# Performance work log

Measured on AMD Instinct MI355X. Metric: run time of the kernel, lower is better.

The kernel has to match this reference:

```python
import jax, jax.numpy as jnp
import numpy as np

B, T, C = 4, 2048, 1024
H, HD = 16, 64          # n_heads, head_dim (C = H*HD)
R = 8                   # LoRA rank
SCALING = 16.0 / R      # alpha / r = 2.0


def setup_inputs() -> dict:
    key = jax.random.key(0)
    ks = jax.random.split(key, 16)
    std_a = 1.0 / np.sqrt(R)  # LoRA A init std (B init is zeros in torch; use randn here for a non-trivial baseline)
    inp = {
        "x":  jax.random.normal(ks[0], (B, T, C), dtype=jnp.float32),
        # per-head stacked projection weights [H, C, HD] (bias=False heads)
        "Wq": jax.random.normal(ks[1], (H, C, HD), dtype=jnp.float32) * 0.02,
        "Wk": jax.random.normal(ks[2], (H, C, HD), dtype=jnp.float32) * 0.02,
        "Wv": jax.random.normal(ks[3], (H, C, HD), dtype=jnp.float32) * 0.02,
        # per-head LoRA factors
        "Aq": jax.random.normal(ks[4], (H, C, R), dtype=jnp.float32) * std_a,
        "Bq": jax.random.normal(ks[5], (H, R, HD), dtype=jnp.float32) * 0.02,
        "Ak": jax.random.normal(ks[6], (H, C, R), dtype=jnp.float32) * std_a,
        "Bk": jax.random.normal(ks[7], (H, R, HD), dtype=jnp.float32) * 0.02,
        "Av": jax.random.normal(ks[8], (H, C, R), dtype=jnp.float32) * std_a,
        "Bv": jax.random.normal(ks[9], (H, R, HD), dtype=jnp.float32) * 0.02,
        # output projection C->C with bias, plus LoRA
        "Wp": jax.random.normal(ks[10], (C, C), dtype=jnp.float32) * 0.02,
        "bp": jnp.zeros((C,), dtype=jnp.float32),
        "Ap": jax.random.normal(ks[11], (C, R), dtype=jnp.float32) * std_a,
        "Bp": jax.random.normal(ks[12], (R, C), dtype=jnp.float32) * 0.02,
    }
    return inp


def _lora_proj(x, W, A, Bm):
    # x: [B,T,C]; W: [H,C,HD]; A: [H,C,R]; Bm: [H,R,HD] -> [B,H,T,HD]
    base = jnp.einsum('btc,hcd->bhtd', x, W)
    lora = jnp.einsum('bhtr,hrd->bhtd', jnp.einsum('btc,hcr->bhtr', x, A), Bm)
    return base + SCALING * lora


def reference(x, Wq, Wk, Wv, Aq, Bq, Ak, Bk, Av, Bv, Wp, bp, Ap, Bp):
    Bsz, Tlen, Cdim = x.shape
    q = _lora_proj(x, Wq, Aq, Bq)  # [B,H,T,HD]
    k = _lora_proj(x, Wk, Ak, Bk)
    v = _lora_proj(x, Wv, Av, Bv)

    scores = jnp.einsum('bhtd,bhsd->bhts', q, k) * (HD ** -0.5)  # [B,H,T,T]
    causal = jnp.tril(jnp.ones((Tlen, Tlen), dtype=bool))
    scores = jnp.where(causal, scores, -jnp.inf)
    weights = jax.nn.softmax(scores, axis=-1)  # dropout p=0 (eval) -> no-op

    out = jnp.einsum('bhts,bhsd->bhtd', weights, v)            # [B,H,T,HD]
    out = out.transpose(0, 2, 1, 3).reshape(Bsz, Tlen, Cdim)   # concat heads

    proj = out @ Wp + bp + SCALING * ((out @ Ap) @ Bp)
    return proj
```

## Files before the change

kernel.cpp:

```cpp
#include <hip/hip_runtime.h>
#include <hip/hip_bf16.h>
#include <stdint.h>

typedef __attribute__((ext_vector_type(4))) float f32x4;
typedef __attribute__((ext_vector_type(8))) short bf16x8;

#define LOG2E 1.44269504088896340736f

__device__ __forceinline__ unsigned short f2bf(float f) {
  union { float f; unsigned u; } c; c.f = f;
  unsigned u = c.u + 0x7FFFu + ((c.u >> 16) & 1u);
  return (unsigned short)(u >> 16);
}

__device__ __forceinline__ void gload_lds16(const void* g, void* l) {
  __builtin_amdgcn_global_load_lds((const __attribute__((address_space(1))) void*)g,
                                   (__attribute__((address_space(3))) void*)l, 16, 0, 0);
}

__global__ __launch_bounds__(256) void cast_x_kernel(const float* __restrict__ x,
                                                     unsigned short* __restrict__ o) {
  int i = blockIdx.x * 256 + threadIdx.x;
  const float4* xv = (const float4*)x;
  float4 a = xv[2 * i], b = xv[2 * i + 1];
  union { uint4 v; unsigned short s[8]; } u;
  u.s[0] = f2bf(a.x); u.s[1] = f2bf(a.y); u.s[2] = f2bf(a.z); u.s[3] = f2bf(a.w);
  u.s[4] = f2bf(b.x); u.s[5] = f2bf(b.y); u.s[6] = f2bf(b.z); u.s[7] = f2bf(b.w);
  ((uint4*)o)[i] = u.v;
}

__global__ __launch_bounds__(256) void fold_head_kernel(const float* __restrict__ W,
                                                        const float* __restrict__ A,
                                                        const float* __restrict__ Bm,
                                                        unsigned short* __restrict__ outT,
                                                        float scale) {
  int h = blockIdx.x, cb = blockIdx.y;
  __shared__ unsigned short tile[64 * 65];
  const float* Wh = W + (size_t)h * 65536;
  const float* Ah = A + (size_t)h * 8192;
  const float* Bh = Bm + (size_t)h * 512;
  int t = threadIdx.x;
  for (int i = 0; i < 16; ++i) {
    int idx = i * 256 + t;
    int cl = idx >> 6, d = idx & 63;
    int c = cb * 64 + cl;
    float acc = 0.f;
#pragma unroll
    for (int r = 0; r < 8; ++r) acc += Ah[c * 8 + r] * Bh[r * 64 + d];
    float val = scale * (Wh[c * 64 + d] + 2.0f * acc);
    tile[cl * 65 + d] = f2bf(val);
  }
  __syncthreads();
  for (int i = 0; i < 16; ++i) {
    int idx = i * 256 + t;
    int d = idx >> 6, cl = idx & 63;
    outT[(size_t)(h * 64 + d) * 1024 + cb * 64 + cl] = tile[cl * 65 + d];
  }
}

__global__ __launch_bounds__(256) void fold_proj_kernel(const float* __restrict__ W,
                                                        const float* __restrict__ A,
                                                        const float* __restrict__ Bm,
                                                        unsigned short* __restrict__ outT) {
  int nb = blockIdx.x, cb = blockIdx.y;
  __shared__ unsigned short tile[64 * 65];
  int t = threadIdx.x;
  for (int i = 0; i < 16; ++i) {
    int idx = i * 256 + t;
    int cl = idx >> 6, d = idx & 63;
    int c = cb * 64 + cl, n = nb * 64 + d;
    float acc = 0.f;
#pragma unroll
    for (int r = 0; r < 8; ++r) acc += A[c * 8 + r] * Bm[r * 1024 + n];
    float val = W[(size_t)c * 1024 + n] + 2.0f * acc;
    tile[cl * 65 + d] = f2bf(val);
  }
  __syncthreads();
  for (int i = 0; i < 16; ++i) {
    int idx = i * 256 + t;
    int d = idx >> 6, cl = idx & 63;
    outT[(size_t)(nb * 64 + d) * 1024 + cb * 64 + cl] = tile[cl * 65 + d];
  }
}

template <int MODE>
__global__ __launch_bounds__(256) void gemm_kernel(const unsigned short* __restrict__ A,
                                                   const unsigned short* __restrict__ B,
                                                   void* __restrict__ Cout,
                                                   const float* __restrict__ bias,
                                                   int M, int N, int K) {
  __shared__ unsigned short lds[8192];
  const int t = threadIdx.x;
  const int m0 = blockIdx.y * 128, n0 = blockIdx.x * 128;
  const int wid = t >> 6, lane = t & 63;
  const int wm = (wid >> 1) * 64, wn = (wid & 1) * 64;
  const int lr = lane & 15, lg = lane >> 4;
  f32x4 acc[4][4];
#pragma unroll
  for (int i = 0; i < 4; ++i)
#pragma unroll
    for (int j = 0; j < 4; ++j) acc[i][j] = (f32x4){0.f, 0.f, 0.f, 0.f};

  for (int k0 = 0; k0 < K; k0 += 32) {
#pragma unroll
    for (int ch = 0; ch < 2; ++ch) {
      int idx = ch * 256 + t;
      int row = idx >> 2, cb = (idx & 3) * 8;
      gload_lds16(A + (size_t)(m0 + row) * K + k0 + cb, &lds[idx * 8]);
    }
#pragma unroll
    for (int ch = 0; ch < 2; ++ch) {
      int idx = ch * 256 + t;
      int row = idx >> 2, cb = (idx & 3) * 8;
      gload_lds16(B + (size_t)(n0 + row) * K + k0 + cb, &lds[4096 + idx * 8]);
    }
    __syncthreads();
    bf16x8 af[4], bfr[4];
#pragma unroll
    for (int i = 0; i < 4; ++i) {
      af[i] = *(const bf16x8*)&lds[(wm + i * 16 + lr) * 32 + lg * 8];
      bfr[i] = *(const bf16x8*)&lds[4096 + (wn + i * 16 + lr) * 32 + lg * 8];
    }
#pragma unroll
    for (int i = 0; i < 4; ++i)
#pragma unroll
      for (int j = 0; j < 4; ++j)
        acc[i][j] = __builtin_amdgcn_mfma_f32_16x16x32_bf16(af[i], bfr[j], acc[i][j], 0, 0, 0);
    __syncthreads();
  }

#pragma unroll
  for (int i = 0; i < 4; ++i) {
#pragma unroll
    for (int r = 0; r < 4; ++r) {
      int row = m0 + wm + i * 16 + lg * 4 + r;
#pragma unroll
      for (int j = 0; j < 4; ++j) {
        int col = n0 + wn + j * 16 + lr;
        float v = acc[i][j][r];
        if (MODE == 0)
          ((unsigned short*)Cout)[(size_t)row * N + col] = f2bf(v);
        else
          ((float*)Cout)[(size_t)row * N + col] = v + bias[col];
      }
    }
  }
}

__global__ __launch_bounds__(256) void vtrans_kernel(const unsigned short* __restrict__ qkv,
                                                     unsigned short* __restrict__ vtb) {
  __shared__ unsigned short tile[64][66];
  const int tt = blockIdx.x, bh = blockIdx.y;
  const int b = bh >> 4, h = bh & 15;
  const size_t srcBase = ((size_t)b * 2048 + tt * 64) * 3072 + 2048 + h * 64;
  const int t = threadIdx.x;
#pragma unroll
  for (int ch = 0; ch < 2; ++ch) {
    int idx = ch * 256 + t;
    int tl = idx >> 3, c = idx & 7;
    *(uint4*)&tile[tl][c * 8] = *(const uint4*)(qkv + srcBase + (size_t)tl * 3072 + c * 8);
  }
  __syncthreads();
#pragma unroll
  for (int ch = 0; ch < 2; ++ch) {
    int idx = ch * 256 + t;
    int d = idx >> 3, tc = idx & 7;
    union { uint4 v; unsigned short s[8]; } u;
#pragma unroll
    for (int j = 0; j < 8; ++j) u.s[j] = tile[tc * 8 + j][d];
    *(uint4*)(vtb + ((size_t)bh * 64 + d) * 2048 + tt * 64 + tc * 8) = u.v;
  }
}

__global__ __launch_bounds__(256) void attn_kernel(const unsigned short* __restrict__ qkv,
                                                   const unsigned short* __restrict__ vtb,
                                                   unsigned short* __restrict__ out) {
  __shared__ __align__(16) char kl[2][8192];
  __shared__ __align__(16) char vt[2][8192];
  __shared__ __align__(16) char pl[8192];
  const int t = threadIdx.x;
  const int wid = t >> 6, lane = t & 63;
  const int lr = lane & 15, lg = lane >> 4;
  const int i = blockIdx.x;
  const int xcd = i & 7, s = i >> 3;
  const int bh = xcd + 8 * (s >> 5);
  const int qtile = 31 - (s & 31);
  const int b = bh >> 4, h = bh & 15;
  const size_t baseRow = (size_t)b * 2048;
  const int nkt = qtile + 1;
  const int q0w = qtile * 64 + wid * 16;
  char* pb = pl + wid * 2048;
  const int swP = ((lr & 1) << 4) | ((lr & 12) << 3);
  const int srow = lane >> 3;
  const int sc = lane & 7;

  const unsigned short* qp = qkv + (baseRow + q0w + lr) * 3072 + h * 64 + lg * 8;
  bf16x8 qf0 = *(const bf16x8*)qp;
  bf16x8 qf1 = *(const bf16x8*)(qp + 32);

  f32x4 acc_o[4];
#pragma unroll
  for (int d = 0; d < 4; ++d) acc_o[d] = (f32x4){0.f, 0.f, 0.f, 0.f};
  float l_acc = 0.f;

  const unsigned short* vrow = vtb + (size_t)bh * 131072;

  auto stage = [&](int kt, int buf) {
#pragma unroll
    for (int ch = 0; ch < 2; ++ch) {
      int kr = ch * 32 + wid * 8 + srow;
      int gc = sc ^ (kr & 7);
      gload_lds16(qkv + (baseRow + kt * 64 + kr) * 3072 + 1024 + h * 64 + gc * 8,
                  &kl[buf][(ch * 256 + t) * 16]);
    }
#pragma unroll
    for (int ch = 0; ch < 2; ++ch) {
      int d = ch * 32 + wid * 8 + srow;
      int gc = sc ^ (((d & 7) ^ (d >> 3)) & 7);
      gload_lds16(vrow + (size_t)d * 2048 + kt * 64 + gc * 8,
                  &vt[buf][(ch * 256 + t) * 16]);
    }
  };

  stage(0, 0);
  __syncthreads();

#pragma unroll 1
  for (int kt = 0; kt < nkt; ++kt) {
    const int cur = kt & 1;
    if (kt + 1 < nkt) stage(kt + 1, cur ^ 1);

    const char* klc = kl[cur];
    f32x4 z[4];
#pragma unroll
    for (int nt = 0; nt < 4; ++nt) {
      int key = nt * 16 + lr;
      const char* kb = klc + key * 128;
      int sw = (key & 7) << 4;
      bf16x8 kf0 = *(const bf16x8*)(kb + ((lg * 16) ^ sw));
      bf16x8 kf1 = *(const bf16x8*)(kb + ((64 + lg * 16) ^ sw));
      f32x4 zz = (f32x4){0.f, 0.f, 0.f, 0.f};
      zz = __builtin_amdgcn_mfma_f32_16x16x32_bf16(kf0, qf0, zz, 0, 0, 0);
      zz = __builtin_amdgcn_mfma_f32_16x16x32_bf16(kf1, qf1, zz, 0, 0, 0);
      z[nt] = zz;
    }
    const bool diag = (kt == qtile);
    const int qg = q0w + lr;
#pragma unroll
    for (int nt = 0; nt < 4; ++nt) {
      union { uint2 v; unsigned short us[4]; } pk;
#pragma unroll
      for (int r = 0; r < 4; ++r) {
        float pv = exp2f(z[nt][r]);
        if (diag) {
          int keyg = kt * 64 + nt * 16 + lg * 4 + r;
          pv = (keyg > qg) ? 0.f : pv;
        }
        l_acc += pv;
        pk.us[r] = f2bf(pv);
      }
      *(uint2*)(pb + lr * 128 + (((nt * 16 + lg * 4) * 2) ^ swP)) = pk.v;
    }
#pragma unroll
    for (int kk = 0; kk < 2; ++kk) {
      bf16x8 pfr = *(const bf16x8*)(pb + lr * 128 + ((kk * 64 + lg * 16) ^ swP));
#pragma unroll
      for (int dt = 0; dt < 4; ++dt) {
        int d = dt * 16 + lr;
        int swv = (((d & 7) ^ ((d >> 3) & 7)) << 4);
        bf16x8 vf = *(const bf16x8*)(vt[cur] + d * 128 + ((kk * 64 + lg * 16) ^ swv));
        acc_o[dt] = __builtin_amdgcn_mfma_f32_16x16x32_bf16(pfr, vf, acc_o[dt], 0, 0, 0);
      }
    }

    __syncthreads();
  }

  float lsum = l_acc;
  lsum += __shfl_xor(lsum, 16);
  lsum += __shfl_xor(lsum, 32);
#pragma unroll
  for (int r = 0; r < 4; ++r) {
    float inv = 1.0f / __shfl(lsum, lg * 4 + r);
    unsigned short* op = out + (baseRow + q0w + lg * 4 + r) * 1024 + h * 64;
#pragma unroll
    for (int dt = 0; dt < 4; ++dt) op[dt * 16 + lr] = f2bf(acc_o[dt][r] * inv);
  }
}

extern "C" void kernel_launch(void* const* d_in, const int* in_sizes, int n_in,
                              void* d_out, int out_size, void* d_ws, size_t ws_size,
                              hipStream_t stream) {
  const float* x = (const float*)d_in[0];
  const float* Wq = (const float*)d_in[1];
  const float* Wk = (const float*)d_in[2];
  const float* Wv = (const float*)d_in[3];
  const float* Aq = (const float*)d_in[4];
  const float* Bq = (const float*)d_in[5];
  const float* Ak = (const float*)d_in[6];
  const float* Bk = (const float*)d_in[7];
  const float* Av = (const float*)d_in[8];
  const float* Bv = (const float*)d_in[9];
  const float* Wp = (const float*)d_in[10];
  const float* bp = (const float*)d_in[11];
  const float* Ap = (const float*)d_in[12];
  const float* Bp = (const float*)d_in[13];

  unsigned short* xb = (unsigned short*)d_ws;
  unsigned short* weff = xb + 8388608;
  unsigned short* wpeff = weff + 3145728;
  unsigned short* qkvb = wpeff + 1048576;
  unsigned short* vtb = qkvb + 25165824;
  unsigned short* attb = xb;

  cast_x_kernel<<<4096, 256, 0, stream>>>(x, xb);
  dim3 fg(16, 16);
  fold_head_kernel<<<fg, 256, 0, stream>>>(Wq, Aq, Bq, weff, 0.125f * LOG2E);
  fold_head_kernel<<<fg, 256, 0, stream>>>(Wk, Ak, Bk, weff + 1048576, 1.0f);
  fold_head_kernel<<<fg, 256, 0, stream>>>(Wv, Av, Bv, weff + 2097152, 1.0f);
  fold_proj_kernel<<<fg, 256, 0, stream>>>(Wp, Ap, Bp, wpeff);

  gemm_kernel<0><<<dim3(24, 64), 256, 0, stream>>>(xb, weff, (void*)qkvb, nullptr, 8192, 3072, 1024);
  vtrans_kernel<<<dim3(32, 64), 256, 0, stream>>>(qkvb, vtb);
  attn_kernel<<<2048, 256, 0, stream>>>(qkvb, vtb, attb);
  gemm_kernel<1><<<dim3(8, 64), 256, 0, stream>>>(attb, wpeff, d_out, bp, 8192, 1024, 1024);
}
```

Measured before the change: 336.4 us.

## Use 256x256 double-buffered GEMM, compute V transposed directly, speed up weight folding

```diff
diff --git a/kernel.cpp b/kernel.cpp
--- a/kernel.cpp
+++ b/kernel.cpp
@@ -35,26 +35,30 @@
                                                         unsigned short* __restrict__ outT,
                                                         float scale) {
   int h = blockIdx.x, cb = blockIdx.y;
-  __shared__ unsigned short tile[64 * 65];
-  const float* Wh = W + (size_t)h * 65536;
-  const float* Ah = A + (size_t)h * 8192;
-  const float* Bh = Bm + (size_t)h * 512;
+  __shared__ float Bs[8][64];
+  __shared__ unsigned short tile[64][65];
   int t = threadIdx.x;
+  if (t < 128) ((float4*)&Bs[0][0])[t] = ((const float4*)(Bm + (size_t)h * 512))[t];
+  __syncthreads();
+  int cl = t >> 2;
+  int c = cb * 64 + cl;
+  int dbase = (t & 3) * 16;
+  float4 a0 = *(const float4*)(A + (size_t)h * 8192 + c * 8);
+  float4 a1 = *(const float4*)(A + (size_t)h * 8192 + c * 8 + 4);
+  const float* Wc = W + (size_t)h * 65536 + (size_t)c * 64;
+#pragma unroll
+  for (int j = 0; j < 16; ++j) {
+    int d = dbase + j;
+    float acc = a0.x * Bs[0][d] + a0.y * Bs[1][d] + a0.z * Bs[2][d] + a0.w * Bs[3][d] +
+                a1.x * Bs[4][d] + a1.y * Bs[5][d] + a1.z * Bs[6][d] + a1.w * Bs[7][d];
+    tile[cl][d] = f2bf(scale * (Wc[d] + 2.0f * acc));
+  }
+  __syncthreads();
+#pragma unroll
   for (int i = 0; i < 16; ++i) {
     int idx = i * 256 + t;
-    int cl = idx >> 6, d = idx & 63;
-    int c = cb * 64 + cl;
-    float acc = 0.f;
-#pragma unroll
-    for (int r = 0; r < 8; ++r) acc += Ah[c * 8 + r] * Bh[r * 64 + d];
-    float val = scale * (Wh[c * 64 + d] + 2.0f * acc);
-    tile[cl * 65 + d] = f2bf(val);
-  }
-  __syncthreads();
-  for (int i = 0; i < 16; ++i) {
-    int idx = i * 256 + t;
-    int d = idx >> 6, cl = idx & 63;
-    outT[(size_t)(h * 64 + d) * 1024 + cb * 64 + cl] = tile[cl * 65 + d];
+    int d = idx >> 6, c2 = idx & 63;
+    outT[(size_t)(h * 64 + d) * 1024 + cb * 64 + c2] = tile[c2][d];
   }
 }
 
@@ -63,112 +67,129 @@
                                                         const float* __restrict__ Bm,
                                                         unsigned short* __restrict__ outT) {
   int nb = blockIdx.x, cb = blockIdx.y;
-  __shared__ unsigned short tile[64 * 65];
+  __shared__ float Bs[8][64];
+  __shared__ unsigned short tile[64][65];
   int t = threadIdx.x;
+  if (t < 128) {
+    int r = t >> 4, dc = t & 15;
+    *(float4*)&Bs[r][dc * 4] = *(const float4*)(Bm + (size_t)r * 1024 + nb * 64 + dc * 4);
+  }
+  __syncthreads();
+  int cl = t >> 2;
+  int c = cb * 64 + cl;
+  int dbase = (t & 3) * 16;
+  float4 a0 = *(const float4*)(A + (size_t)c * 8);
+  float4 a1 = *(const float4*)(A + (size_t)c * 8 + 4);
+  const float* Wc = W + (size_t)c * 1024 + nb * 64;
+#pragma unroll
+  for (int j = 0; j < 16; ++j) {
+    int d = dbase + j;
+    float acc = a0.x * Bs[0][d] + a0.y * Bs[1][d] + a0.z * Bs[2][d] + a0.w * Bs[3][d] +
+                a1.x * Bs[4][d] + a1.y * Bs[5][d] + a1.z * Bs[6][d] + a1.w * Bs[7][d];
+    tile[cl][d] = f2bf(Wc[d] + 2.0f * acc);
+  }
+  __syncthreads();
+#pragma unroll
   for (int i = 0; i < 16; ++i) {
     int idx = i * 256 + t;
-    int cl = idx >> 6, d = idx & 63;
-    int c = cb * 64 + cl, n = nb * 64 + d;
-    float acc = 0.f;
-#pragma unroll
-    for (int r = 0; r < 8; ++r) acc += A[c * 8 + r] * Bm[r * 1024 + n];
-    float val = W[(size_t)c * 1024 + n] + 2.0f * acc;
-    tile[cl * 65 + d] = f2bf(val);
-  }
-  __syncthreads();
-  for (int i = 0; i < 16; ++i) {
-    int idx = i * 256 + t;
-    int d = idx >> 6, cl = idx & 63;
-    outT[(size_t)(nb * 64 + d) * 1024 + cb * 64 + cl] = tile[cl * 65 + d];
+    int d = idx >> 6, c2 = idx & 63;
+    outT[(size_t)(nb * 64 + d) * 1024 + cb * 64 + c2] = tile[c2][d];
   }
 }
 
 template <int MODE>
-__global__ __launch_bounds__(256) void gemm_kernel(const unsigned short* __restrict__ A,
-                                                   const unsigned short* __restrict__ B,
-                                                   void* __restrict__ Cout,
-                                                   const float* __restrict__ bias,
-                                                   int M, int N, int K) {
-  __shared__ unsigned short lds[8192];
+__global__ __launch_bounds__(512) void gemm256_kernel(const unsigned short* __restrict__ A,
+                                                      const unsigned short* __restrict__ B,
+                                                      void* __restrict__ Cout,
+                                                      const float* __restrict__ bias,
+                                                      int M, int N, int K) {
+  __shared__ __align__(16) unsigned short lds[2][32768];
   const int t = threadIdx.x;
-  const int m0 = blockIdx.y * 128, n0 = blockIdx.x * 128;
-  const int wid = t >> 6, lane = t & 63;
-  const int wm = (wid >> 1) * 64, wn = (wid & 1) * 64;
+  const int lane = t & 63;
+  const int wid = t >> 6;
+  const int wm = wid >> 2, wn = wid & 3;
   const int lr = lane & 15, lg = lane >> 4;
-  f32x4 acc[4][4];
-#pragma unroll
-  for (int i = 0; i < 4; ++i)
+  const int m0 = blockIdx.y * 256, n0 = blockIdx.x * 256;
+
+  f32x4 acc[8][4];
+#pragma unroll
+  for (int i = 0; i < 8; ++i)
 #pragma unroll
     for (int j = 0; j < 4; ++j) acc[i][j] = (f32x4){0.f, 0.f, 0.f, 0.f};
 
-  for (int k0 = 0; k0 < K; k0 += 32) {
-#pragma unroll
-    for (int ch = 0; ch < 2; ++ch) {
-      int idx = ch * 256 + t;
-      int row = idx >> 2, cb = (idx & 3) * 8;
-      gload_lds16(A + (size_t)(m0 + row) * K + k0 + cb, &lds[idx * 8]);
-    }
-#pragma unroll
-    for (int ch = 0; ch < 2; ++ch) {
-      int idx = ch * 256 + t;
-      int row = idx >> 2, cb = (idx & 3) * 8;
-      gload_lds16(B + (size_t)(n0 + row) * K + k0 + cb, &lds[4096 + idx * 8]);
+  const int srow = t >> 3;
+  const int schk = t & 7;
+
+  auto stage_all = [&](int buf, int kt) {
+    const int k0 = kt * 64;
+#pragma unroll
+    for (int hh = 0; hh < 4; ++hh) {
+      const unsigned short* src = (hh < 2) ? A : B;
+      const int r0 = ((hh < 2) ? m0 : n0) + (hh & 1) * 128;
+      char* dst = (char*)lds[buf] + (hh >= 2 ? 32768 : 0) + (hh & 1) * 16384;
+#pragma unroll
+      for (int i = 0; i < 2; ++i) {
+        int row = i * 64 + srow;
+        int gc = schk ^ (row & 7);
+        gload_lds16(src + (size_t)(r0 + row) * K + k0 + gc * 8, dst + i * 8192 + t * 16);
+      }
+    }
+  };
+
+  stage_all(0, 0);
+  __syncthreads();
+
+  const int NT = K >> 6;
+#pragma unroll 1
+  for (int kt = 0; kt < NT; ++kt) {
+    const int cur = kt & 1;
+    const char* Ab = (const char*)lds[cur];
+    const char* Bb = (const char*)lds[cur] + 32768;
+#pragma unroll
+    for (int p = 0; p < 4; ++p) {
+      if (p == 0 && kt + 1 < NT) stage_all(cur ^ 1, kt + 1);
+      const int mh = p >> 1, nh = p & 1;
+#pragma unroll
+      for (int kk = 0; kk < 2; ++kk) {
+        bf16x8 af[4], bfr[2];
+#pragma unroll
+        for (int fm = 0; fm < 4; ++fm) {
+          int row = wm * 128 + mh * 64 + fm * 16 + lr;
+          af[fm] = *(const bf16x8*)(Ab + row * 128 + (((kk * 4 + lg) ^ (row & 7)) * 16));
+        }
+#pragma unroll
+        for (int fn = 0; fn < 2; ++fn) {
+          int row = wn * 64 + nh * 32 + fn * 16 + lr;
+          bfr[fn] = *(const bf16x8*)(Bb + row * 128 + (((kk * 4 + lg) ^ (row & 7)) * 16));
+        }
+        __builtin_amdgcn_s_setprio(1);
+#pragma unroll
+        for (int fm = 0; fm < 4; ++fm)
+#pragma unroll
+          for (int fn = 0; fn < 2; ++fn)
+            acc[mh * 4 + fm][nh * 2 + fn] =
+                __builtin_amdgcn_mfma_f32_16x16x32_bf16(af[fm], bfr[fn], acc[mh * 4 + fm][nh * 2 + fn], 0, 0, 0);
+        __builtin_amdgcn_s_setprio(0);
+      }
     }
     __syncthreads();
-    bf16x8 af[4], bfr[4];
-#pragma unroll
-    for (int i = 0; i < 4; ++i) {
-      af[i] = *(const bf16x8*)&lds[(wm + i * 16 + lr) * 32 + lg * 8];
-      bfr[i] = *(const bf16x8*)&lds[4096 + (wn + i * 16 + lr) * 32 + lg * 8];
-    }
-#pragma unroll
-    for (int i = 0; i < 4; ++i)
-#pragma unroll
-      for (int j = 0; j < 4; ++j)
-        acc[i][j] = __builtin_amdgcn_mfma_f32_16x16x32_bf16(af[i], bfr[j], acc[i][j], 0, 0, 0);
-    __syncthreads();
-  }
-
-#pragma unroll
-  for (int i = 0; i < 4; ++i) {
+  }
+
+#pragma unroll
+  for (int fm = 0; fm < 8; ++fm) {
 #pragma unroll
     for (int r = 0; r < 4; ++r) {
-      int row = m0 + wm + i * 16 + lg * 4 + r;
-#pragma unroll
-      for (int j = 0; j < 4; ++j) {
-        int col = n0 + wn + j * 16 + lr;
-        float v = acc[i][j][r];
+      int row = m0 + wm * 128 + fm * 16 + lg * 4 + r;
+#pragma unroll
+      for (int fn = 0; fn < 4; ++fn) {
+        int col = n0 + wn * 64 + fn * 16 + lr;
+        float v = acc[fm][fn][r];
         if (MODE == 0)
           ((unsigned short*)Cout)[(size_t)row * N + col] = f2bf(v);
         else
           ((float*)Cout)[(size_t)row * N + col] = v + bias[col];
       }
     }
-  }
-}
-
-__global__ __launch_bounds__(256) void vtrans_kernel(const unsigned short* __restrict__ qkv,
-                                                     unsigned short* __restrict__ vtb) {
-  __shared__ unsigned short tile[64][66];
-  const int tt = blockIdx.x, bh = blockIdx.y;
-  const int b = bh >> 4, h = bh & 15;
-  const size_t srcBase = ((size_t)b * 2048 + tt * 64) * 3072 + 2048 + h * 64;
-  const int t = threadIdx.x;
-#pragma unroll
-  for (int ch = 0; ch < 2; ++ch) {
-    int idx = ch * 256 + t;
-    int tl = idx >> 3, c = idx & 7;
-    *(uint4*)&tile[tl][c * 8] = *(const uint4*)(qkv + srcBase + (size_t)tl * 3072 + c * 8);
-  }
-  __syncthreads();
-#pragma unroll
-  for (int ch = 0; ch < 2; ++ch) {
-    int idx = ch * 256 + t;
-    int d = idx >> 3, tc = idx & 7;
-    union { uint4 v; unsigned short s[8]; } u;
-#pragma unroll
-    for (int j = 0; j < 8; ++j) u.s[j] = tile[tc * 8 + j][d];
-    *(uint4*)(vtb + ((size_t)bh * 64 + d) * 2048 + tt * 64 + tc * 8) = u.v;
   }
 }
 
@@ -194,7 +215,7 @@
   const int srow = lane >> 3;
   const int sc = lane & 7;
 
-  const unsigned short* qp = qkv + (baseRow + q0w + lr) * 3072 + h * 64 + lg * 8;
+  const unsigned short* qp = qkv + (baseRow + q0w + lr) * 2048 + h * 64 + lg * 8;
   bf16x8 qf0 = *(const bf16x8*)qp;
   bf16x8 qf1 = *(const bf16x8*)(qp + 32);
 
@@ -203,21 +224,21 @@
   for (int d = 0; d < 4; ++d) acc_o[d] = (f32x4){0.f, 0.f, 0.f, 0.f};
   float l_acc = 0.f;
 
-  const unsigned short* vrow = vtb + (size_t)bh * 131072;
+  const unsigned short* vrow = vtb + (size_t)(h * 64) * 8192 + baseRow;
 
   auto stage = [&](int kt, int buf) {
 #pragma unroll
     for (int ch = 0; ch < 2; ++ch) {
       int kr = ch * 32 + wid * 8 + srow;
       int gc = sc ^ (kr & 7);
-      gload_lds16(qkv + (baseRow + kt * 64 + kr) * 3072 + 1024 + h * 64 + gc * 8,
+      gload_lds16(qkv + (baseRow + kt * 64 + kr) * 2048 + 1024 + h * 64 + gc * 8,
                   &kl[buf][(ch * 256 + t) * 16]);
     }
 #pragma unroll
     for (int ch = 0; ch < 2; ++ch) {
       int d = ch * 32 + wid * 8 + srow;
       int gc = sc ^ (((d & 7) ^ (d >> 3)) & 7);
-      gload_lds16(vrow + (size_t)d * 2048 + kt * 64 + gc * 8,
+      gload_lds16(vrow + (size_t)d * 8192 + kt * 64 + gc * 8,
                   &vt[buf][(ch * 256 + t) * 16]);
     }
   };
@@ -272,7 +293,6 @@
         acc_o[dt] = __builtin_amdgcn_mfma_f32_16x16x32_bf16(pfr, vf, acc_o[dt], 0, 0, 0);
       }
     }
-
     __syncthreads();
   }
 
@@ -308,20 +328,21 @@
 
   unsigned short* xb = (unsigned short*)d_ws;
   unsigned short* weff = xb + 8388608;
-  unsigned short* wpeff = weff + 3145728;
-  unsigned short* qkvb = wpeff + 1048576;
-  unsigned short* vtb = qkvb + 25165824;
+  unsigned short* weffV = weff + 2097152;
+  unsigned short* wpeff = weffV + 1048576;
+  unsigned short* qkb = wpeff + 1048576;
+  unsigned short* vtb = qkb + 16777216;
   unsigned short* attb = xb;
 
   cast_x_kernel<<<4096, 256, 0, stream>>>(x, xb);
   dim3 fg(16, 16);
   fold_head_kernel<<<fg, 256, 0, stream>>>(Wq, Aq, Bq, weff, 0.125f * LOG2E);
   fold_head_kernel<<<fg, 256, 0, stream>>>(Wk, Ak, Bk, weff + 1048576, 1.0f);
-  fold_head_kernel<<<fg, 256, 0, stream>>>(Wv, Av, Bv, weff + 2097152, 1.0f);
+  fold_head_kernel<<<fg, 256, 0, stream>>>(Wv, Av, Bv, weffV, 1.0f);
   fold_proj_kernel<<<fg, 256, 0, stream>>>(Wp, Ap, Bp, wpeff);
 
-  gemm_kernel<0><<<dim3(24, 64), 256, 0, stream>>>(xb, weff, (void*)qkvb, nullptr, 8192, 3072, 1024);
-  vtrans_kernel<<<dim3(32, 64), 256, 0, stream>>>(qkvb, vtb);
-  attn_kernel<<<2048, 256, 0, stream>>>(qkvb, vtb, attb);
-  gemm_kernel<1><<<dim3(8, 64), 256, 0, stream>>>(attb, wpeff, d_out, bp, 8192, 1024, 1024);
-}
+  gemm256_kernel<0><<<dim3(8, 32), 512, 0, stream>>>(xb, weff, (void*)qkb, nullptr, 8192, 2048, 1024);
+  gemm256_kernel<0><<<dim3(32, 4), 512, 0, stream>>>(weffV, xb, (void*)vtb, nullptr, 1024, 8192, 1024);
+  attn_kernel<<<2048, 256, 0, stream>>>(qkb, vtb, attb);
+  gemm256_kernel<1><<<dim3(4, 32), 512, 0, stream>>>(attb, wpeff, d_out, bp, 8192, 1024, 1024);
+}
```

Measured after the change: 329.4 us. 1.02x faster.
